# Performance work log

Hardware: AMD Instinct MI355X
Metric: run time of the kernel (lower is better)

Reference implementation:

```python
import jax, jax.numpy as jnp
import numpy as np

B, S, D_MODEL, D_FF = 8, 1024, 512, 2048
NCAT, NSUB, TOPK = 8, 8, 2
E = NCAT * NSUB            # 64 experts
CAP = 1024


def setup_inputs() -> dict:
    key = jax.random.key(0)
    ks = jax.random.split(key, 6)
    hidden = jax.random.normal(ks[0], (B, S, D_MODEL), jnp.float32)
    cat_indices = jax.random.randint(ks[1], (B, S, TOPK), 0, NCAT)
    sub_indices = jax.random.randint(ks[2], (B, S, TOPK), 0, NSUB)
    weights = jax.random.uniform(ks[3], (B, S, TOPK), jnp.float32)
    # Stacked per-expert MLP params (Expert = Linear -> GELU -> Linear, dropout off in eval)
    W1 = jax.random.normal(ks[4], (E, D_MODEL, D_FF), jnp.float32) / np.sqrt(D_MODEL).astype(np.float32)
    b1 = jnp.zeros((E, D_FF), jnp.float32)
    W2 = jax.random.normal(ks[5], (E, D_FF, D_MODEL), jnp.float32) / np.sqrt(D_FF).astype(np.float32)
    b2 = jnp.zeros((E, D_MODEL), jnp.float32)
    return dict(hidden=hidden, cat_indices=cat_indices, sub_indices=sub_indices,
                weights=weights, W1=W1, b1=b1, W2=W2, b2=b2)


def _moe_forward(hidden, cat_indices, sub_indices, weights, W1, b1, W2, b2):
    Bq, Sq, d = hidden.shape
    K = cat_indices.shape[-1]
    T = Bq * Sq            # tokens
    A = T * K              # (token, k) routing assignments
    x = hidden.reshape(T, d)
    eid = (cat_indices * NSUB + sub_indices).reshape(A).astype(jnp.int32)  # flat expert id
    wf = weights.reshape(A)
    tok = jnp.arange(A, dtype=jnp.int32) // K  # token index per assignment

    # position of each assignment within its expert's capacity buffer
    oh = jax.nn.one_hot(eid, E, dtype=jnp.int32)                     # [A, E]
    pos = jnp.take_along_axis(jnp.cumsum(oh, axis=0) - 1,
                              eid[:, None].astype(jnp.int32), axis=1)[:, 0]
    valid = (pos < CAP).astype(hidden.dtype)

    # dispatch: gather tokens into [E, CAP, d] buffer (overflow dropped; CAP sized to avoid it)
    buf = jnp.zeros((E, CAP, d), hidden.dtype).at[eid, pos].set(x[tok], mode='drop')

    # grouped expert MLP: Linear -> GELU -> Linear
    h = jax.nn.gelu(jnp.einsum('ecd,edf->ecf', buf, W1) + b1[:, None, :], approximate=False)
    yb = jnp.einsum('ecf,efd->ecd', h, W2) + b2[:, None, :]          # [E, CAP, d]

    # combine: gather each assignment's expert output, weight it, scatter-add over tokens
    pc = jnp.minimum(pos, CAP - 1)
    ya = yb[eid, pc] * (wf * valid)[:, None]                          # [A, d]
    out = jnp.zeros((T, d), hidden.dtype).at[tok].add(ya)
    return out.reshape(Bq, Sq, d)


def reference(hidden, cat_indices, sub_indices, weights, W1, b1, W2, b2):
    return _moe_forward(hidden, cat_indices, sub_indices, weights, W1, b1, W2, b2)
```

## Files before the change

kernel.cpp:

```cpp
#include <hip/hip_runtime.h>
#include <hip/hip_bf16.h>
#include <cstdint>
#include <cstddef>

#define TOKENS 8192
#define ASSIGN 16384
#define DM     512
#define DFF    2048
#define NEXP   64
#define NSUB_  8
#define CAP2   512
#define BK     64
#define BMT    256

typedef __bf16 bf16;
typedef __bf16 bf16x4 __attribute__((ext_vector_type(4)));
typedef __bf16 bf16x8 __attribute__((ext_vector_type(8)));
typedef float  f32x4  __attribute__((ext_vector_type(4)));

__global__ void k_route(const int* __restrict__ cat, const int* __restrict__ sub,
                        int* __restrict__ count, int* __restrict__ slot_of) {
    int a = blockIdx.x * 256 + threadIdx.x;
    if (a >= ASSIGN) return;
    int e = cat[a] * NSUB_ + sub[a];
    int s = atomicAdd(&count[e], 1);
    slot_of[a] = (s < CAP2) ? (e * CAP2 + s) : -1;
}

__global__ void k_gather(const float* __restrict__ hidden, const int* __restrict__ slot_of,
                         bf16* __restrict__ xg) {
    int a = blockIdx.x * 4 + (threadIdx.x >> 6);
    int t = threadIdx.x & 63;
    int r = slot_of[a];
    if (r < 0) return;
    int tok = a >> 1;
    const f32x4* src = (const f32x4*)(hidden + (size_t)tok * DM);
    f32x4 v0 = src[t * 2], v1 = src[t * 2 + 1];
    bf16x8 o;
    o[0] = (bf16)v0[0]; o[1] = (bf16)v0[1]; o[2] = (bf16)v0[2]; o[3] = (bf16)v0[3];
    o[4] = (bf16)v1[0]; o[5] = (bf16)v1[1]; o[6] = (bf16)v1[2]; o[7] = (bf16)v1[3];
    *(bf16x8*)(xg + (size_t)r * DM + t * 8) = o;
}

__device__ inline float gelu_tanh(float x) {
    float s2 = 1.5957691216057308f * x * (1.0f + 0.044715f * x * x);
    float z = __expf(-fabsf(s2));
    float sig = 1.0f / (1.0f + z);
    return (s2 >= 0.0f) ? x * sig : x * (1.0f - sig);
}

__device__ inline void gload_lds16(const void* g, void* l) {
    __builtin_amdgcn_global_load_lds((const __attribute__((address_space(1))) void*)g,
                                     (__attribute__((address_space(3))) void*)l, 16, 0, 0);
}

template <bool GELU>
__global__ __launch_bounds__(512, 4)
void k_gemm(const bf16* __restrict__ A, const float* __restrict__ W,
            const float* __restrict__ bias, bf16* __restrict__ C,
            const int* __restrict__ count, int N, int K, int ntn) {
    __shared__ __align__(16) char As[BMT * 128];
    __shared__ __align__(16) char Bs[128 * 128];

    int nwg = gridDim.x;
    int lg = (int)(blockIdx.x & 7) * (nwg >> 3) + (int)(blockIdx.x >> 3);
    int e = lg / (2 * ntn);
    int rem = lg - e * 2 * ntn;
    int ntile = rem >> 1, mtile = rem & 1;

    int mc = count[e]; if (mc > CAP2) mc = CAP2;
    if (mtile * BMT >= mc) return;
    int tid = threadIdx.x, wave = tid >> 6, lane = tid & 63;
    int wm = wave >> 1, wn = wave & 1;

    const char*  Ag = (const char*)(A + (size_t)(e * CAP2 + mtile * BMT) * K);
    const float* Wg = W + (size_t)e * K * N + (size_t)ntile * 128;

    int kq = ((lane >> 3) & 7) | ((wave & 1) << 3);
    int nq = (lane & 7) | (((wave >> 1) & 3) << 3);

    f32x4 br[4];
    auto issueB = [&](int kt) {
        const float* p = Wg + (size_t)(kt * BK + kq * 4) * N + nq * 4;
        br[0] = *(const f32x4*)(p);
        br[1] = *(const f32x4*)(p + N);
        br[2] = *(const f32x4*)(p + 2 * (size_t)N);
        br[3] = *(const f32x4*)(p + 3 * (size_t)N);
    };
    auto writeB = [&]() {
#pragma unroll
        for (int c = 0; c < 4; c++) {
            int n = nq * 4 + c;
            bf16x4 v;
#pragma unroll
            for (int j = 0; j < 4; j++) v[j] = (bf16)br[j][c];
            *(bf16x4*)(Bs + n * 128 + ((kq * 8) ^ ((n & 7) << 4))) = v;
        }
    };
    auto issueA = [&](int kt) {
#pragma unroll
        for (int i = 0; i < 4; i++) {
            int chunk = i * 8 + wave;
            int d = chunk * 1024 + lane * 16;
            int row = d >> 7;
            int col = (d & 127) ^ ((row & 7) << 4);
            gload_lds16(Ag + (size_t)row * (2 * K) + (size_t)kt * 128 + col,
                        As + chunk * 1024);
        }
    };

    f32x4 acc[4][4];
#pragma unroll
    for (int i = 0; i < 4; i++)
#pragma unroll
        for (int j = 0; j < 4; j++) acc[i][j] = f32x4{0.f, 0.f, 0.f, 0.f};

    issueB(0);
    int nK = K >> 6;
    for (int kt = 0; kt < nK; kt++) {
        issueA(kt);
        asm volatile("s_waitcnt vmcnt(0)" ::: "memory");
        writeB();
        if (kt + 1 < nK) issueB(kt + 1);
        asm volatile("s_waitcnt lgkmcnt(0)" ::: "memory");
        __builtin_amdgcn_s_barrier();
        __builtin_amdgcn_sched_barrier(0);
#pragma unroll
        for (int ks = 0; ks < 2; ks++) {
            bf16x8 af[4], bfv[4];
#pragma unroll
            for (int mi = 0; mi < 4; mi++) {
                int row = wm * 64 + mi * 16 + (lane & 15);
                af[mi] = *(const bf16x8*)(As + row * 128 +
                         ((ks * 64 + (lane >> 4) * 16) ^ ((row & 7) << 4)));
            }
#pragma unroll
            for (int ni = 0; ni < 4; ni++) {
                int n = wn * 64 + ni * 16 + (lane & 15);
                bfv[ni] = *(const bf16x8*)(Bs + n * 128 +
                          ((ks * 64 + (lane >> 4) * 16) ^ ((n & 7) << 4)));
            }
#pragma unroll
            for (int mi = 0; mi < 4; mi++)
#pragma unroll
                for (int ni = 0; ni < 4; ni++)
                    acc[mi][ni] = __builtin_amdgcn_mfma_f32_16x16x32_bf16(
                        af[mi], bfv[ni], acc[mi][ni], 0, 0, 0);
        }
        __builtin_amdgcn_sched_barrier(0);
        __builtin_amdgcn_s_barrier();
    }

#pragma unroll
    for (int mi = 0; mi < 4; mi++) {
        int rowb = wm * 64 + mi * 16 + ((lane >> 4) << 2);
#pragma unroll
        for (int ni = 0; ni < 4; ni++) {
            int col = ntile * 128 + wn * 64 + ni * 16 + (lane & 15);
            float bv = bias[e * N + col];
#pragma unroll
            for (int r = 0; r < 4; r++) {
                float v = acc[mi][ni][r] + bv;
                if (GELU) v = gelu_tanh(v);
                int grow = e * CAP2 + mtile * BMT + rowb + r;
                C[(size_t)grow * N + col] = (bf16)v;
            }
        }
    }
}

__global__ void k_combine(const float* __restrict__ wts, const int* __restrict__ slot_of,
                          const bf16* __restrict__ y, float* __restrict__ out) {
    int tok = blockIdx.x * 4 + (threadIdx.x >> 6);
    int t = threadIdx.x & 63;
    float acc[8] = {0, 0, 0, 0, 0, 0, 0, 0};
#pragma unroll
    for (int k = 0; k < 2; k++) {
        int a = tok * 2 + k;
        int r = slot_of[a];
        if (r >= 0) {
            float w = wts[a];
            bf16x8 v = *(const bf16x8*)(y + (size_t)r * DM + t * 8);
#pragma unroll
            for (int j = 0; j < 8; j++) acc[j] += w * (float)v[j];
        }
    }
    f32x4* o = (f32x4*)(out + (size_t)tok * DM + t * 8);
    o[0] = f32x4{acc[0], acc[1], acc[2], acc[3]};
    o[1] = f32x4{acc[4], acc[5], acc[6], acc[7]};
}

extern "C" void kernel_launch(void* const* d_in, const int* in_sizes, int n_in,
                              void* d_out, int out_size, void* d_ws, size_t ws_size,
                              hipStream_t stream) {
    const float* hidden = (const float*)d_in[0];
    const int*   cat    = (const int*)d_in[1];
    const int*   sub    = (const int*)d_in[2];
    const float* wts    = (const float*)d_in[3];
    const float* W1     = (const float*)d_in[4];
    const float* b1     = (const float*)d_in[5];
    const float* W2     = (const float*)d_in[6];
    const float* b2     = (const float*)d_in[7];
    float* out = (float*)d_out;

    char* ws = (char*)d_ws;
    size_t off = 0;
    bf16* hbuf = (bf16*)(ws + off); off += (size_t)NEXP * CAP2 * DFF * 2;
    bf16* xg   = (bf16*)(ws + off); off += (size_t)NEXP * CAP2 * DM * 2;
    bf16* y    = xg;
    int* count   = (int*)(ws + off); off += 256;
    int* slot_of = (int*)(ws + off); off += (size_t)ASSIGN * 4;

    hipMemsetAsync(count, 0, 256, stream);
    k_route<<<ASSIGN / 256, 256, 0, stream>>>(cat, sub, count, slot_of);
    k_gather<<<ASSIGN / 4, 256, 0, stream>>>(hidden, slot_of, xg);

    k_gemm<true><<<dim3(NEXP * 16 * 2), 512, 0, stream>>>(
        xg, W1, b1, hbuf, count, DFF, DM, 16);

    k_gemm<false><<<dim3(NEXP * 4 * 2), 512, 0, stream>>>(
        hbuf, W2, b2, y, count, DM, DFF, 4);

    k_combine<<<TOKENS / 4, 256, 0, stream>>>(wts, slot_of, y, out);
}
```

Baseline: 295.4 us.

## Fuse weighted combine into second expert GEMM epilogue via atomic scatter-add

The second GEMM's epilogue now scatters bias-added outputs straight into the float output. It looks up the assignment through a new inverse slot table built during routing, scales by the routing weight and uses atomicAdd. This removes the combine kernel and the bf16 round trip of the expert output buffer. In exchange it needs an extra memset of the output, adds per-element float atomics with scattered addresses, and makes accumulation order nondeterministic.

```diff
diff --git a/kernel.cpp b/kernel.cpp
--- a/kernel.cpp
+++ b/kernel.cpp
@@ -19,12 +19,18 @@
 typedef float  f32x4  __attribute__((ext_vector_type(4)));
 
 __global__ void k_route(const int* __restrict__ cat, const int* __restrict__ sub,
-                        int* __restrict__ count, int* __restrict__ slot_of) {
+                        int* __restrict__ count, int* __restrict__ slot_of,
+                        int* __restrict__ inv) {
     int a = blockIdx.x * 256 + threadIdx.x;
     if (a >= ASSIGN) return;
     int e = cat[a] * NSUB_ + sub[a];
     int s = atomicAdd(&count[e], 1);
-    slot_of[a] = (s < CAP2) ? (e * CAP2 + s) : -1;
+    if (s < CAP2) {
+        slot_of[a] = e * CAP2 + s;
+        inv[e * CAP2 + s] = a;
+    } else {
+        slot_of[a] = -1;
+    }
 }
 
 __global__ void k_gather(const float* __restrict__ hidden, const int* __restrict__ slot_of,
@@ -54,11 +60,13 @@
                                      (__attribute__((address_space(3))) void*)l, 16, 0, 0);
 }
 
-template <bool GELU>
+template <bool GELU, bool SCATTER>
 __global__ __launch_bounds__(512, 4)
 void k_gemm(const bf16* __restrict__ A, const float* __restrict__ W,
             const float* __restrict__ bias, bf16* __restrict__ C,
-            const int* __restrict__ count, int N, int K, int ntn) {
+            const int* __restrict__ count, int N, int K, int ntn,
+            const int* __restrict__ inv, const float* __restrict__ wts,
+            float* __restrict__ out) {
     __shared__ __align__(16) char As[BMT * 128];
     __shared__ __align__(16) char Bs[128 * 128];
 
@@ -154,40 +162,36 @@
 #pragma unroll
     for (int mi = 0; mi < 4; mi++) {
         int rowb = wm * 64 + mi * 16 + ((lane >> 4) << 2);
-#pragma unroll
-        for (int ni = 0; ni < 4; ni++) {
-            int col = ntile * 128 + wn * 64 + ni * 16 + (lane & 15);
-            float bv = bias[e * N + col];
+        if (SCATTER) {
 #pragma unroll
             for (int r = 0; r < 4; r++) {
-                float v = acc[mi][ni][r] + bv;
-                if (GELU) v = gelu_tanh(v);
-                int grow = e * CAP2 + mtile * BMT + rowb + r;
-                C[(size_t)grow * N + col] = (bf16)v;
+                int srow = mtile * BMT + rowb + r;
+                if (srow >= mc) continue;
+                int a = inv[e * CAP2 + srow];
+                float w = wts[a];
+                int tok = a >> 1;
+#pragma unroll
+                for (int ni = 0; ni < 4; ni++) {
+                    int col = ntile * 128 + wn * 64 + ni * 16 + (lane & 15);
+                    float v = acc[mi][ni][r] + bias[e * N + col];
+                    atomicAdd(&out[(size_t)tok * DM + col], w * v);
+                }
+            }
+        } else {
+#pragma unroll
+            for (int ni = 0; ni < 4; ni++) {
+                int col = ntile * 128 + wn * 64 + ni * 16 + (lane & 15);
+                float bv = bias[e * N + col];
+#pragma unroll
+                for (int r = 0; r < 4; r++) {
+                    float v = acc[mi][ni][r] + bv;
+                    if (GELU) v = gelu_tanh(v);
+                    int grow = e * CAP2 + mtile * BMT + rowb + r;
+                    C[(size_t)grow * N + col] = (bf16)v;
+                }
             }
         }
     }
-}
-
-__global__ void k_combine(const float* __restrict__ wts, const int* __restrict__ slot_of,
-                          const bf16* __restrict__ y, float* __restrict__ out) {
-    int tok = blockIdx.x * 4 + (threadIdx.x >> 6);
-    int t = threadIdx.x & 63;
-    float acc[8] = {0, 0, 0, 0, 0, 0, 0, 0};
-#pragma unroll
-    for (int k = 0; k < 2; k++) {
-        int a = tok * 2 + k;
-        int r = slot_of[a];
-        if (r >= 0) {
-            float w = wts[a];
-            bf16x8 v = *(const bf16x8*)(y + (size_t)r * DM + t * 8);
-#pragma unroll
-            for (int j = 0; j < 8; j++) acc[j] += w * (float)v[j];
-        }
-    }
-    f32x4* o = (f32x4*)(out + (size_t)tok * DM + t * 8);
-    o[0] = f32x4{acc[0], acc[1], acc[2], acc[3]};
-    o[1] = f32x4{acc[4], acc[5], acc[6], acc[7]};
 }
 
 extern "C" void kernel_launch(void* const* d_in, const int* in_sizes, int n_in,
@@ -207,19 +211,18 @@
     size_t off = 0;
     bf16* hbuf = (bf16*)(ws + off); off += (size_t)NEXP * CAP2 * DFF * 2;
     bf16* xg   = (bf16*)(ws + off); off += (size_t)NEXP * CAP2 * DM * 2;
-    bf16* y    = xg;
     int* count   = (int*)(ws + off); off += 256;
     int* slot_of = (int*)(ws + off); off += (size_t)ASSIGN * 4;
+    int* inv     = (int*)(ws + off); off += (size_t)NEXP * CAP2 * 4;
 
     hipMemsetAsync(count, 0, 256, stream);
-    k_route<<<ASSIGN / 256, 256, 0, stream>>>(cat, sub, count, slot_of);
+    hipMemsetAsync(out, 0, (size_t)out_size * 4, stream);
+    k_route<<<ASSIGN / 256, 256, 0, stream>>>(cat, sub, count, slot_of, inv);
     k_gather<<<ASSIGN / 4, 256, 0, stream>>>(hidden, slot_of, xg);
 
-    k_gemm<true><<<dim3(NEXP * 16 * 2), 512, 0, stream>>>(
-        xg, W1, b1, hbuf, count, DFF, DM, 16);
-
-    k_gemm<false><<<dim3(NEXP * 4 * 2), 512, 0, stream>>>(
-        hbuf, W2, b2, y, count, DM, DFF, 4);
-
-    k_combine<<<TOKENS / 4, 256, 0, stream>>>(wts, slot_of, y, out);
-}
+    k_gemm<true, false><<<dim3(NEXP * 16 * 2), 512, 0, stream>>>(
+        xg, W1, b1, hbuf, count, DFF, DM, 16, nullptr, nullptr, nullptr);
+
+    k_gemm<false, true><<<dim3(NEXP * 4 * 2), 512, 0, stream>>>(
+        hbuf, W2, b2, nullptr, count, DM, DFF, 4, inv, wts, out);
+}
```

New measurement: 331.1 us. 12.1% more time.
